# Kernel tuning notes

Measured on AMD Instinct MI355X. Metric: run time of the kernel, lower is better.

The kernel has to match this reference:

```python
import jax, jax.numpy as jnp
import numpy as np

B, SQ, SK, H, HK, D = 2, 2048, 2048, 32, 8, 128

def setup_inputs() -> dict:
    key = jax.random.key(0)
    k1, k2, k3 = jax.random.split(key, 3)
    q = jax.random.normal(k1, (B, SQ, H, D), dtype=jnp.float32)
    kv = jax.random.normal(k2, (B, SK, 2, HK, D), dtype=jnp.float32)
    # ragged valid lengths per batch (True = keep)
    lengths = jax.random.randint(k3, (B,), SK // 2, SK + 1)
    key_padding_mask = jnp.arange(SK)[None, :] < lengths[:, None]
    return {"q": q, "kv": kv, "key_padding_mask": key_padding_mask}

def reference(q, kv, key_padding_mask):
    b, sq, h, d = q.shape
    sk, hk = kv.shape[1], kv.shape[3]
    if hk != h:
        kv = jnp.repeat(kv, h // hk, axis=3)  # GQA: (hkv g) contiguous repeat
    k, v = kv[:, :, 0], kv[:, :, 1]  # (B, Sk, H, D)
    scale = 1.0 / jnp.sqrt(jnp.asarray(d, dtype=q.dtype))
    scores = jnp.einsum('bthd,bshd->bhts', q, k * scale)  # (B, H, Sq, Sk)
    pad = jnp.where(key_padding_mask, 0.0, -10000.0).astype(scores.dtype)
    scores = scores + pad[:, None, None, :]
    row = jnp.arange(sq)[:, None]
    col = jnp.arange(sk)[None, :]
    sk_valid = key_padding_mask.sum(-1)[:, None, None, None]  # (B,1,1,1)
    causal_mask = col[None, None] > row[None, None] + sk_valid - sq
    scores = jnp.where(causal_mask, jnp.asarray(-10000.0, scores.dtype), scores)
    attention = jax.nn.softmax(scores, axis=-1)
    # dropout p=0.0 -> identity
    return jnp.einsum('bhts,bshd->bthd', attention, v)  # (B, Sq, H, D)
```

## Files before the change

kernel.cpp:

```cpp
#include <hip/hip_runtime.h>
#include <hip/hip_bf16.h>
#include <cstdint>
#include <cstddef>

constexpr int B_ = 2, SQ_ = 2048, SK_ = 2048, H_ = 32, HK_ = 8, D_ = 128;
constexpr float SCALE_ = 0.08838834764831845f;
constexpr float QSCALE_ = 0.12751874f;
constexpr float THR_ = 11.5f;

typedef __attribute__((ext_vector_type(4))) float f32x4;
typedef __attribute__((ext_vector_type(8))) short bf16x8;
typedef __attribute__((ext_vector_type(4))) short bf16x4;

__device__ __forceinline__ unsigned short f2bf(float f) {
  union { float f; uint32_t u; } v; v.f = f;
  uint32_t u = v.u;
  return (unsigned short)((u + 0x7FFFu + ((u >> 16) & 1u)) >> 16);
}

__device__ __forceinline__ unsigned short cvt_bf16(float x) {
  __hip_bfloat16 h = __float2bfloat16(x);
  return *reinterpret_cast<unsigned short*>(&h);
}

__device__ __forceinline__ float exp2_fast(float x) {
  float r;
  asm volatile("v_exp_f32 %0, %1" : "=v"(r) : "v"(x));
  return r;
}

__device__ __forceinline__ void gload16(const void* g, void* l) {
  __builtin_amdgcn_global_load_lds((const __attribute__((address_space(1))) void*)g,
                                   (__attribute__((address_space(3))) void*)l, 16, 0, 0);
}

__global__ void skv_kernel(const void* __restrict__ mask, int* __restrict__ skv_out) {
  const int b = blockIdx.x;
  const int tid = threadIdx.x;
  __shared__ int red[256];
  const uint32_t* mw = (const uint32_t*)mask;
  const uint32_t w0 = mw[0], w1 = mw[1];
  int cnt = 0;
  if (w0 > 1u) {
    const uint8_t* m = (const uint8_t*)mask + (size_t)b * SK_;
    for (int s = tid; s < SK_; s += 256) cnt += (m[s] != 0);
  } else if (w1 == 0u) {
    const uint32_t* m = mw + (size_t)b * SK_ * 2;
    for (int s = tid; s < SK_; s += 256) cnt += (m[2 * s] != 0);
  } else {
    const int* m = (const int*)mask + (size_t)b * SK_;
    for (int s = tid; s < SK_; s += 256) cnt += (m[s] != 0);
  }
  red[tid] = cnt;
  __syncthreads();
  for (int o = 128; o > 0; o >>= 1) {
    if (tid < o) red[tid] += red[tid + o];
    __syncthreads();
  }
  if (tid == 0) skv_out[b] = red[0];
}

__global__ void meanv_kernel(const float* __restrict__ kv, float* __restrict__ meanv) {
  const int blk = blockIdx.x;
  const int chunk = blk & 15;
  const int hk = (blk >> 4) & 7;
  const int b = blk >> 7;
  const int d = threadIdx.x;
  float sum = 0.0f;
  for (int i = 0; i < 128; ++i) {
    const int s = chunk * 128 + i;
    sum += kv[((((size_t)b * SK_ + s) * 2 + 1) * HK_ + hk) * D_ + d];
  }
  atomicAdd(meanv + ((size_t)b * HK_ + hk) * D_ + d, sum * (1.0f / (float)SK_));
}

__global__ void convk(const float* __restrict__ kv, unsigned short* __restrict__ Kb) {
  const int b = blockIdx.z, hk = blockIdx.y;
  const int s = blockIdx.x * 16 + (threadIdx.x >> 4);
  const int dc = (threadIdx.x & 15) * 8;
  const float* src = kv + ((((size_t)b * SK_ + s) * 2 + 0) * HK_ + hk) * D_ + dc;
  f32x4 a0 = *(const f32x4*)src;
  f32x4 a1 = *(const f32x4*)(src + 4);
  bf16x8 t;
  t[0] = (short)f2bf(a0[0]); t[1] = (short)f2bf(a0[1]);
  t[2] = (short)f2bf(a0[2]); t[3] = (short)f2bf(a0[3]);
  t[4] = (short)f2bf(a1[0]); t[5] = (short)f2bf(a1[1]);
  t[6] = (short)f2bf(a1[2]); t[7] = (short)f2bf(a1[3]);
  *(bf16x8*)(Kb + ((size_t)(b * HK_ + hk) * SK_ + s) * D_ + dc) = t;
}

__global__ void convvt(const float* __restrict__ kv, unsigned short* __restrict__ VTb) {
  const int b = blockIdx.z, hk = blockIdx.y;
  const int s0 = blockIdx.x * 64;
  const int d = threadIdx.x & 127;
  const int sg = threadIdx.x >> 7;
  unsigned short vals[32];
#pragma unroll
  for (int i = 0; i < 32; ++i) {
    const int s = s0 + sg * 32 + i;
    vals[i] = f2bf(kv[((((size_t)b * SK_ + s) * 2 + 1) * HK_ + hk) * D_ + d]);
  }
  unsigned short* dst = VTb + ((size_t)(b * HK_ + hk) * D_ + d) * SK_ + s0 + sg * 32;
#pragma unroll
  for (int c = 0; c < 4; ++c) {
    bf16x8 t;
#pragma unroll
    for (int i = 0; i < 8; ++i) t[i] = (short)vals[c * 8 + i];
    *(bf16x8*)(dst + c * 8) = t;
  }
}

__global__ __launch_bounds__(256, 2)
void flash15(const float* __restrict__ q, const unsigned short* __restrict__ Kb,
             const unsigned short* __restrict__ VTb, const int* __restrict__ skv_arr,
             const float* __restrict__ meanv, float* __restrict__ out,
             int* __restrict__ work_ctr) {
  const int tid = threadIdx.x;
  const int w = tid >> 6, l = tid & 63, lg = l >> 4, lr = l & 15;

  __shared__ char smem[65536];
  char* kc0 = smem;          char* vc0 = smem + 16384;
  char* kn0 = smem + 32768;  char* vn0 = smem + 49152;

  const int NITEMS = (SQ_ / 32) * HK_ * B_;

  for (;;) {
    if (tid == 0) *(volatile int*)smem = atomicAdd(work_ctr, 1);
    __syncthreads();
    const int r = *(volatile int*)smem;
    __syncthreads();
    if (r >= NITEMS) break;

    const int qt = 63 - (r >> 4);
    const int hk = (r >> 1) & 7;
    const int b = r & 1;
    const int h = hk * 4 + w;
    const int t0 = qt * 32;
    const int skv = skv_arr[b];

    char* kc = kc0; char* kn = kn0; char* vc = vc0; char* vn = vn0;

    bf16x8 qf[2][4];
#pragma unroll
    for (int rb = 0; rb < 2; ++rb) {
      const int trow = t0 + rb * 16 + lr;
      const float* qp = q + (((size_t)b * SQ_ + trow) * H_ + h) * D_;
#pragma unroll
      for (int kk = 0; kk < 4; ++kk) {
        f32x4 a0 = *(const f32x4*)(qp + kk * 32 + lg * 8);
        f32x4 a1 = *(const f32x4*)(qp + kk * 32 + lg * 8 + 4);
        bf16x8 t;
        t[0] = (short)f2bf(a0[0] * QSCALE_); t[1] = (short)f2bf(a0[1] * QSCALE_);
        t[2] = (short)f2bf(a0[2] * QSCALE_); t[3] = (short)f2bf(a0[3] * QSCALE_);
        t[4] = (short)f2bf(a1[0] * QSCALE_); t[5] = (short)f2bf(a1[1] * QSCALE_);
        t[6] = (short)f2bf(a1[2] * QSCALE_); t[7] = (short)f2bf(a1[3] * QSCALE_);
        qf[rb][kk] = t;
      }
    }

    f32x4 acc0[8], acc1[8];
#pragma unroll
    for (int i = 0; i < 8; ++i) { acc0[i] = (f32x4)0.0f; acc1[i] = (f32x4)0.0f; }
    float m_[2], l_[2];
#pragma unroll
    for (int rb = 0; rb < 2; ++rb) { m_[rb] = -1e30f; l_[rb] = 0.0f; }

    int n_allowed = t0 + 31 + skv - SQ_ + 1;
    if (n_allowed > skv) n_allowed = skv;
    const int nt = (n_allowed > 0) ? ((n_allowed + 63) >> 6) : 0;

    const char* kgb = (const char*)Kb + ((size_t)(b * HK_ + hk)) * SK_ * D_ * 2;
    const char* vgb = (const char*)VTb + ((size_t)(b * HK_ + hk)) * (size_t)D_ * SK_ * 2;

    auto stage = [&](char* kdst, char* vdst, int s0) {
      const char* kt = kgb + (size_t)s0 * 256;
#pragma unroll
      for (int i = 0; i < 4; ++i) {
        const int c8 = w * 4 + i;
        const int beta = c8 * 1024 + l * 16;
        const int row = beta >> 8;
        gload16(kt + (beta ^ ((row & 7) << 4)), kdst + c8 * 1024);
      }
      const char* vt = vgb + s0 * 2;
#pragma unroll
      for (int i = 0; i < 4; ++i) {
        const int c8 = w * 4 + i;
        const int beta = c8 * 1024 + l * 16;
        const int lam = beta ^ (((beta >> 7) & 7) << 4);
        const int d = lam >> 7, keyb = lam & 127;
        gload16(vt + (size_t)d * (SK_ * 2) + keyb, vdst + c8 * 1024);
      }
    };

    asm volatile("s_waitcnt vmcnt(0)" ::: "memory");
    if (nt > 0) stage(kc, vc, 0);

    for (int j = 0; j < nt; ++j) {
      if (j + 1 < nt) {
        stage(kn, vn, (j + 1) * 64);
        asm volatile("s_waitcnt vmcnt(8)" ::: "memory");
      } else {
        asm volatile("s_waitcnt vmcnt(0)" ::: "memory");
      }
      __builtin_amdgcn_s_barrier();

      const int s0 = j * 64;
      f32x4 sc[2][4];
#pragma unroll
      for (int c = 0; c < 4; ++c) { sc[0][c] = (f32x4)0.0f; sc[1][c] = (f32x4)0.0f; }
      __builtin_amdgcn_s_setprio(1);
#pragma unroll
      for (int c = 0; c < 4; ++c) {
        const int row = c * 16 + lr;
        const int kx = (row & 7) << 4;
#pragma unroll
        for (int kk = 0; kk < 4; ++kk) {
          const int byte = (row << 8) + ((kk * 32 + lg * 8) << 1);
          bf16x8 kf = *(const bf16x8*)(kc + (byte ^ kx));
          sc[0][c] = __builtin_amdgcn_mfma_f32_16x16x32_bf16(kf, qf[0][kk], sc[0][c], 0, 0, 0);
          sc[1][c] = __builtin_amdgcn_mfma_f32_16x16x32_bf16(kf, qf[1][kk], sc[1][c], 0, 0, 0);
        }
      }
      __builtin_amdgcn_s_setprio(0);

      const int kbase = s0 + (lg << 2);
#pragma unroll
      for (int rb = 0; rb < 2; ++rb) {
        const int lim_min = t0 + rb * 16 + skv - SQ_;
        if (s0 + 63 > lim_min) {
          const int lim = t0 + rb * 16 + lr + skv - SQ_;
#pragma unroll
          for (int c = 0; c < 4; ++c)
#pragma unroll
            for (int rr = 0; rr < 4; ++rr)
              if (kbase + c * 16 + rr > lim) sc[rb][c][rr] = -1e30f;
        }
      }

      float mx0 = sc[0][0][0], mx1 = sc[1][0][0];
#pragma unroll
      for (int c = 0; c < 4; ++c)
#pragma unroll
        for (int rr = 0; rr < 4; ++rr) {
          mx0 = fmaxf(mx0, sc[0][c][rr]);
          mx1 = fmaxf(mx1, sc[1][c][rr]);
        }
      const float worst = fmaxf(mx0 - m_[0], mx1 - m_[1]);
      if (!__all(worst <= THR_)) {
        float fm[2] = {mx0, mx1};
        float al_[2];
#pragma unroll
        for (int rb = 0; rb < 2; ++rb) {
          float t = fmaxf(fm[rb], __shfl_xor(fm[rb], 16));
          t = fmaxf(t, __shfl_xor(t, 32));
          const float mn = fmaxf(m_[rb], t);
          al_[rb] = exp2_fast(m_[rb] - mn);
          m_[rb] = mn;
          l_[rb] *= al_[rb];
        }
        float alq0[4], alq1[4];
#pragma unroll
        for (int rr = 0; rr < 4; ++rr) {
          alq0[rr] = __shfl(al_[0], lg * 4 + rr, 16);
          alq1[rr] = __shfl(al_[1], lg * 4 + rr, 16);
        }
#pragma unroll
        for (int dd = 0; dd < 8; ++dd)
#pragma unroll
          for (int rr = 0; rr < 4; ++rr) { acc0[dd][rr] *= alq0[rr]; acc1[dd][rr] *= alq1[rr]; }
      }

      bf16x8 pa8[2][2];
#pragma unroll
      for (int rb = 0; rb < 2; ++rb) {
        const float mm = m_[rb];
        float ps = 0.0f;
#pragma unroll
        for (int c = 0; c < 4; ++c) {
          const int c2 = c >> 1, half = (c & 1) * 4;
#pragma unroll
          for (int rr = 0; rr < 4; ++rr) {
            const float pv = exp2_fast(sc[rb][c][rr] - mm);
            ps += pv;
            pa8[rb][c2][half + rr] = (short)cvt_bf16(pv);
          }
        }
        l_[rb] += ps;
      }

      __builtin_amdgcn_s_setprio(1);
#pragma unroll
      for (int dd = 0; dd < 8; ++dd) {
        const int d = dd * 16 + lr;
        const int swz = (d & 7) << 4;
#pragma unroll
        for (int c2 = 0; c2 < 2; ++c2) {
          const int base = d * 128 + c2 * 64 + lg * 8;
          bf16x4 vlo = *(const bf16x4*)(vc + (base ^ swz));
          bf16x4 vhi = *(const bf16x4*)(vc + ((base + 32) ^ swz));
          bf16x8 b8 = {vlo[0], vlo[1], vlo[2], vlo[3], vhi[0], vhi[1], vhi[2], vhi[3]};
          acc0[dd] = __builtin_amdgcn_mfma_f32_16x16x32_bf16(pa8[0][c2], b8, acc0[dd], 0, 0, 0);
          acc1[dd] = __builtin_amdgcn_mfma_f32_16x16x32_bf16(pa8[1][c2], b8, acc1[dd], 0, 0, 0);
        }
      }
      __builtin_amdgcn_s_setprio(0);
      asm volatile("" ::: "memory");
      __builtin_amdgcn_s_barrier();
      { char* t = kc; kc = kn; kn = t; t = vc; vc = vn; vn = t; }
    }

    const float* mp = meanv + ((size_t)(b * HK_ + hk)) * D_;
#pragma unroll
    for (int rb = 0; rb < 2; ++rb) {
      const f32x4* acc = rb ? acc1 : acc0;
      float lsum = l_[rb] + __shfl_xor(l_[rb], 16);
      lsum += __shfl_xor(lsum, 32);
#pragma unroll
      for (int rr = 0; rr < 4; ++rr) {
        const float lq = __shfl(lsum, lg * 4 + rr, 16);
        const int t_r = t0 + rb * 16 + lg * 4 + rr;
        const bool deg = (t_r + skv - SQ_) < 0;
        const float inv = 1.0f / lq;
        float* op = out + (((size_t)b * SQ_ + t_r) * H_ + h) * D_;
#pragma unroll
        for (int dd = 0; dd < 8; ++dd) {
          const int d = dd * 16 + lr;
          op[d] = deg ? mp[d] : acc[dd][rr] * inv;
        }
      }
    }
    __syncthreads();
  }
}

extern "C" void kernel_launch(void* const* d_in, const int* in_sizes, int n_in,
                              void* d_out, int out_size, void* d_ws, size_t ws_size,
                              hipStream_t stream) {
  const float* q = (const float*)d_in[0];
  const float* kv = (const float*)d_in[1];
  const void* mask = d_in[2];
  float* out = (float*)d_out;

  const size_t KB_OFF = 0;
  const size_t VT_OFF = 8ull * 1024 * 1024;
  const size_t MV_OFF = 16ull * 1024 * 1024;
  unsigned short* Kb = (unsigned short*)((char*)d_ws + KB_OFF);
  unsigned short* VTb = (unsigned short*)((char*)d_ws + VT_OFF);
  float* meanv = (float*)((char*)d_ws + MV_OFF);
  int* skv = (int*)((char*)d_ws + MV_OFF + 8192);
  int* work_ctr = (int*)((char*)d_ws + MV_OFF + 8192 + 64);

  hipMemsetAsync((char*)d_ws + MV_OFF, 0, 8192 + 128, stream);
  skv_kernel<<<B_, 256, 0, stream>>>(mask, skv);
  convk<<<dim3(SK_ / 16, HK_, B_), 256, 0, stream>>>(kv, Kb);
  convvt<<<dim3(SK_ / 64, HK_, B_), 256, 0, stream>>>(kv, VTb);
  meanv_kernel<<<B_ * HK_ * 16, 128, 0, stream>>>(kv, meanv);
  flash15<<<dim3(512), 256, 0, stream>>>(q, Kb, VTb, skv, meanv, out, work_ctr);
}
```

Measured before the change: 156.2 us.

## Single-buffer V in LDS, raise occupancy to three blocks per CU

Shared memory drops from 64KB to 48KB by double-buffering only K. V is now loaded into a single buffer at the start of each iteration and overlaps the QK^T MFMAs, with an extra wait and barrier before the PV stage. Launch bounds rise to 3 blocks per CU and the persistent grid grows to 768. The softmax and PV work is restructured per row block, which lowers register pressure. The cost is that V loads are exposed within each iteration and an extra barrier is added, in exchange for more resident waves to hide latency.

```diff
diff --git a/kernel.cpp b/kernel.cpp
--- a/kernel.cpp
+++ b/kernel.cpp
@@ -4,7 +4,6 @@
 #include <cstddef>
 
 constexpr int B_ = 2, SQ_ = 2048, SK_ = 2048, H_ = 32, HK_ = 8, D_ = 128;
-constexpr float SCALE_ = 0.08838834764831845f;
 constexpr float QSCALE_ = 0.12751874f;
 constexpr float THR_ = 11.5f;
 
@@ -110,17 +109,18 @@
   }
 }
 
-__global__ __launch_bounds__(256, 2)
-void flash15(const float* __restrict__ q, const unsigned short* __restrict__ Kb,
+__global__ __launch_bounds__(256, 3)
+void flash18(const float* __restrict__ q, const unsigned short* __restrict__ Kb,
              const unsigned short* __restrict__ VTb, const int* __restrict__ skv_arr,
              const float* __restrict__ meanv, float* __restrict__ out,
              int* __restrict__ work_ctr) {
   const int tid = threadIdx.x;
   const int w = tid >> 6, l = tid & 63, lg = l >> 4, lr = l & 15;
 
-  __shared__ char smem[65536];
-  char* kc0 = smem;          char* vc0 = smem + 16384;
-  char* kn0 = smem + 32768;  char* vn0 = smem + 49152;
+  __shared__ char smem[49152];
+  char* kb0 = smem;
+  char* kb1 = smem + 16384;
+  char* vb  = smem + 32768;
 
   const int NITEMS = (SQ_ / 32) * HK_ * B_;
 
@@ -137,8 +137,6 @@
     const int h = hk * 4 + w;
     const int t0 = qt * 32;
     const int skv = skv_arr[b];
-
-    char* kc = kc0; char* kn = kn0; char* vc = vc0; char* vn = vn0;
 
     bf16x8 qf[2][4];
 #pragma unroll
@@ -172,7 +170,7 @@
     const char* kgb = (const char*)Kb + ((size_t)(b * HK_ + hk)) * SK_ * D_ * 2;
     const char* vgb = (const char*)VTb + ((size_t)(b * HK_ + hk)) * (size_t)D_ * SK_ * 2;
 
-    auto stage = [&](char* kdst, char* vdst, int s0) {
+    auto stage_k = [&](char* kdst, int s0) {
       const char* kt = kgb + (size_t)s0 * 256;
 #pragma unroll
       for (int i = 0; i < 4; ++i) {
@@ -181,30 +179,35 @@
         const int row = beta >> 8;
         gload16(kt + (beta ^ ((row & 7) << 4)), kdst + c8 * 1024);
       }
-      const char* vt = vgb + s0 * 2;
+    };
+    auto stage_v = [&](int s0) {
+      const char* vt = vgb + (size_t)s0 * 2;
 #pragma unroll
       for (int i = 0; i < 4; ++i) {
         const int c8 = w * 4 + i;
         const int beta = c8 * 1024 + l * 16;
         const int lam = beta ^ (((beta >> 7) & 7) << 4);
         const int d = lam >> 7, keyb = lam & 127;
-        gload16(vt + (size_t)d * (SK_ * 2) + keyb, vdst + c8 * 1024);
+        gload16(vt + (size_t)d * (SK_ * 2) + keyb, vb + c8 * 1024);
       }
     };
 
     asm volatile("s_waitcnt vmcnt(0)" ::: "memory");
-    if (nt > 0) stage(kc, vc, 0);
+    if (nt > 0) stage_k(kb0, 0);
 
     for (int j = 0; j < nt; ++j) {
-      if (j + 1 < nt) {
-        stage(kn, vn, (j + 1) * 64);
-        asm volatile("s_waitcnt vmcnt(8)" ::: "memory");
-      } else {
-        asm volatile("s_waitcnt vmcnt(0)" ::: "memory");
-      }
+      char* kcur = (j & 1) ? kb1 : kb0;
+      char* knext = (j & 1) ? kb0 : kb1;
+      const int s0 = j * 64;
+
+      stage_v(s0);
+      const bool more = (j + 1 < nt);
+      if (more) stage_k(knext, (j + 1) * 64);
+
+      if (more) { asm volatile("s_waitcnt vmcnt(8)" ::: "memory"); }
+      else      { asm volatile("s_waitcnt vmcnt(4)" ::: "memory"); }
       __builtin_amdgcn_s_barrier();
 
-      const int s0 = j * 64;
       f32x4 sc[2][4];
 #pragma unroll
       for (int c = 0; c < 4; ++c) { sc[0][c] = (f32x4)0.0f; sc[1][c] = (f32x4)0.0f; }
@@ -216,16 +219,23 @@
 #pragma unroll
         for (int kk = 0; kk < 4; ++kk) {
           const int byte = (row << 8) + ((kk * 32 + lg * 8) << 1);
-          bf16x8 kf = *(const bf16x8*)(kc + (byte ^ kx));
+          bf16x8 kf = *(const bf16x8*)(kcur + (byte ^ kx));
           sc[0][c] = __builtin_amdgcn_mfma_f32_16x16x32_bf16(kf, qf[0][kk], sc[0][c], 0, 0, 0);
           sc[1][c] = __builtin_amdgcn_mfma_f32_16x16x32_bf16(kf, qf[1][kk], sc[1][c], 0, 0, 0);
         }
       }
       __builtin_amdgcn_s_setprio(0);
 
+      if (more) { asm volatile("s_waitcnt vmcnt(4)" ::: "memory"); }
+      else      { asm volatile("s_waitcnt vmcnt(0)" ::: "memory"); }
+      __builtin_amdgcn_s_barrier();
+
       const int kbase = s0 + (lg << 2);
 #pragma unroll
       for (int rb = 0; rb < 2; ++rb) {
+        f32x4* scr = sc[rb];
+        f32x4* accr = rb ? acc1 : acc0;
+
         const int lim_min = t0 + rb * 16 + skv - SQ_;
         if (s0 + 63 > lim_min) {
           const int lim = t0 + rb * 16 + lr + skv - SQ_;
@@ -233,80 +243,66 @@
           for (int c = 0; c < 4; ++c)
 #pragma unroll
             for (int rr = 0; rr < 4; ++rr)
-              if (kbase + c * 16 + rr > lim) sc[rb][c][rr] = -1e30f;
-        }
-      }
-
-      float mx0 = sc[0][0][0], mx1 = sc[1][0][0];
-#pragma unroll
-      for (int c = 0; c < 4; ++c)
-#pragma unroll
-        for (int rr = 0; rr < 4; ++rr) {
-          mx0 = fmaxf(mx0, sc[0][c][rr]);
-          mx1 = fmaxf(mx1, sc[1][c][rr]);
-        }
-      const float worst = fmaxf(mx0 - m_[0], mx1 - m_[1]);
-      if (!__all(worst <= THR_)) {
-        float fm[2] = {mx0, mx1};
-        float al_[2];
-#pragma unroll
-        for (int rb = 0; rb < 2; ++rb) {
-          float t = fmaxf(fm[rb], __shfl_xor(fm[rb], 16));
-          t = fmaxf(t, __shfl_xor(t, 32));
-          const float mn = fmaxf(m_[rb], t);
-          al_[rb] = exp2_fast(m_[rb] - mn);
+              if (kbase + c * 16 + rr > lim) scr[c][rr] = -1e30f;
+        }
+
+        float mx = scr[0][0];
+#pragma unroll
+        for (int c = 0; c < 4; ++c)
+#pragma unroll
+          for (int rr = 0; rr < 4; ++rr) mx = fmaxf(mx, scr[c][rr]);
+        if (!__all(mx - m_[rb] <= THR_)) {
+          float fm = fmaxf(mx, __shfl_xor(mx, 16));
+          fm = fmaxf(fm, __shfl_xor(fm, 32));
+          const float mn = fmaxf(m_[rb], fm);
+          const float al = exp2_fast(m_[rb] - mn);
           m_[rb] = mn;
-          l_[rb] *= al_[rb];
-        }
-        float alq0[4], alq1[4];
-#pragma unroll
-        for (int rr = 0; rr < 4; ++rr) {
-          alq0[rr] = __shfl(al_[0], lg * 4 + rr, 16);
-          alq1[rr] = __shfl(al_[1], lg * 4 + rr, 16);
-        }
-#pragma unroll
-        for (int dd = 0; dd < 8; ++dd)
-#pragma unroll
-          for (int rr = 0; rr < 4; ++rr) { acc0[dd][rr] *= alq0[rr]; acc1[dd][rr] *= alq1[rr]; }
-      }
-
-      bf16x8 pa8[2][2];
-#pragma unroll
-      for (int rb = 0; rb < 2; ++rb) {
-        const float mm = m_[rb];
-        float ps = 0.0f;
-#pragma unroll
-        for (int c = 0; c < 4; ++c) {
-          const int c2 = c >> 1, half = (c & 1) * 4;
-#pragma unroll
-          for (int rr = 0; rr < 4; ++rr) {
-            const float pv = exp2_fast(sc[rb][c][rr] - mm);
-            ps += pv;
-            pa8[rb][c2][half + rr] = (short)cvt_bf16(pv);
+          l_[rb] *= al;
+          float alq[4];
+#pragma unroll
+          for (int rr = 0; rr < 4; ++rr) alq[rr] = __shfl(al, lg * 4 + rr, 16);
+#pragma unroll
+          for (int dd = 0; dd < 8; ++dd)
+#pragma unroll
+            for (int rr = 0; rr < 4; ++rr) accr[dd][rr] *= alq[rr];
+        }
+
+        bf16x8 pa8[2];
+        {
+          const float mm = m_[rb];
+          float ps = 0.0f;
+#pragma unroll
+          for (int c = 0; c < 4; ++c) {
+            const int c2 = c >> 1, half = (c & 1) * 4;
+#pragma unroll
+            for (int rr = 0; rr < 4; ++rr) {
+              const float pv = exp2_fast(scr[c][rr] - mm);
+              ps += pv;
+              pa8[c2][half + rr] = (short)cvt_bf16(pv);
+            }
           }
-        }
-        l_[rb] += ps;
-      }
-
-      __builtin_amdgcn_s_setprio(1);
-#pragma unroll
-      for (int dd = 0; dd < 8; ++dd) {
-        const int d = dd * 16 + lr;
-        const int swz = (d & 7) << 4;
-#pragma unroll
-        for (int c2 = 0; c2 < 2; ++c2) {
-          const int base = d * 128 + c2 * 64 + lg * 8;
-          bf16x4 vlo = *(const bf16x4*)(vc + (base ^ swz));
-          bf16x4 vhi = *(const bf16x4*)(vc + ((base + 32) ^ swz));
-          bf16x8 b8 = {vlo[0], vlo[1], vlo[2], vlo[3], vhi[0], vhi[1], vhi[2], vhi[3]};
-          acc0[dd] = __builtin_amdgcn_mfma_f32_16x16x32_bf16(pa8[0][c2], b8, acc0[dd], 0, 0, 0);
-          acc1[dd] = __builtin_amdgcn_mfma_f32_16x16x32_bf16(pa8[1][c2], b8, acc1[dd], 0, 0, 0);
-        }
-      }
-      __builtin_amdgcn_s_setprio(0);
+          l_[rb] += ps;
+        }
+
+        __builtin_amdgcn_s_setprio(1);
+#pragma unroll
+        for (int dd = 0; dd < 8; ++dd) {
+          const int d = dd * 16 + lr;
+          const int swz = (d & 7) << 4;
+#pragma unroll
+          for (int c2 = 0; c2 < 2; ++c2) {
+            const int base = d * 128 + c2 * 64 + lg * 8;
+            bf16x4 vlo = *(const bf16x4*)(vb + (base ^ swz));
+            bf16x4 vhi = *(const bf16x4*)(vb + ((base + 32) ^ swz));
+            bf16x8 b8 = {vlo[0], vlo[1], vlo[2], vlo[3], vhi[0], vhi[1], vhi[2], vhi[3]};
+            accr[dd] = __builtin_amdgcn_mfma_f32_16x16x32_bf16(pa8[c2], b8, accr[dd], 0, 0, 0);
+          }
+        }
+        __builtin_amdgcn_s_setprio(0);
+      }
+
       asm volatile("" ::: "memory");
       __builtin_amdgcn_s_barrier();
-      { char* t = kc; kc = kn; kn = t; t = vc; vc = vn; vn = t; }
     }
 
     const float* mp = meanv + ((size_t)(b * HK_ + hk)) * D_;
@@ -355,5 +351,5 @@
   convk<<<dim3(SK_ / 16, HK_, B_), 256, 0, stream>>>(kv, Kb);
   convvt<<<dim3(SK_ / 64, HK_, B_), 256, 0, stream>>>(kv, VTb);
   meanv_kernel<<<B_ * HK_ * 16, 128, 0, stream>>>(kv, meanv);
-  flash15<<<dim3(512), 256, 0, stream>>>(q, Kb, VTb, skv, meanv, out, work_ctr);
-}
+  flash18<<<dim3(768), 256, 0, stream>>>(q, Kb, VTb, skv, meanv, out, work_ctr);
+}
```

New measurement: 588.4 us. 277% more time.
